# Kernel tuning notes

Hardware: AMD Instinct MI355X
Metric: run time of the kernel (lower is better)

The kernel has to match this reference:

```python
import jax, jax.numpy as jnp
import numpy as np

HEAD_DIM = 128
NUM_Q_HEAD = 32
NUM_KV_HEAD = 8
GROUP_SIZE = 128
EPS = 1e-5
WINDOW = 512
CAP = 50.0
CLIP_L, CLIP_R = -0.01, 1.01
SCALE = 1.0 / np.sqrt(HEAD_DIM)
NEG = -1e9


def group_rmsnorm(x, gamma, gsz, eps):
    # x: [B, S, H]; per-group RMS over contiguous chunks of size gsz, then learned scale
    b, s, h = x.shape
    xg = x.reshape(b, s, h // gsz, gsz)
    rms = jnp.sqrt(jnp.mean(xg * xg, axis=-1, keepdims=True) + eps)
    return (xg / rms).reshape(b, s, h) * gamma


def setup_inputs() -> dict:
    key = jax.random.key(0)
    k1, k2, k3, k4, k5 = jax.random.split(key, 5)
    B, S = 2, 2048
    q = jax.random.normal(k1, (B, S, NUM_Q_HEAD, HEAD_DIM), dtype=jnp.float32)
    k = jax.random.normal(k2, (B, S, NUM_KV_HEAD, HEAD_DIM), dtype=jnp.float32)
    v = jax.random.normal(k3, (B, S, NUM_KV_HEAD, HEAD_DIM), dtype=jnp.float32)
    # GroupRMSNorm weights ~ U(init_range) = U(-1, 1)
    gamma_q = jax.random.uniform(k4, (NUM_Q_HEAD * HEAD_DIM,), dtype=jnp.float32, minval=-1.0, maxval=1.0)
    gamma_k = jax.random.uniform(k5, (NUM_KV_HEAD * HEAD_DIM,), dtype=jnp.float32, minval=-1.0, maxval=1.0)
    return {"q": q, "k": k, "v": v, "gamma_q": gamma_q, "gamma_k": gamma_k}


def reference(q, k, v, gamma_q, gamma_k):
    B, Sq, Hq, D = q.shape
    Sk, Hkv = k.shape[1], k.shape[2]
    # QK GroupRMSNorm on flattened hidden dim
    qn = group_rmsnorm(q.reshape(B, Sq, Hq * D), gamma_q, GROUP_SIZE, EPS).reshape(B, Sq, Hq, D)
    kn = group_rmsnorm(k.reshape(B, Sk, Hkv * D), gamma_k, GROUP_SIZE, EPS).reshape(B, Sk, Hkv, D)
    # GQA: repeat_interleave kv heads to match q heads
    rep = Hq // Hkv
    kr = jnp.repeat(kn, rep, axis=2)
    vr = jnp.repeat(v, rep, axis=2)
    # scores: [B, H, Sq, Sk]
    logits = jnp.einsum('bqhd,bkhd->bhqk', qn, kr) * SCALE
    # softmax capping (temperature path skipped when cap is set)
    logits = jnp.tanh(logits / CAP) * CAP
    # causal + sliding-window mask (aligned at sequence end)
    i = jnp.arange(Sq)[:, None]
    j = jnp.arange(Sk)[None, :]
    pos = i + (Sk - Sq)
    allowed = (j <= pos) & (pos - j <= WINDOW)
    logits = jnp.where(allowed, logits, NEG)
    probs = jax.nn.softmax(logits.astype(jnp.float32), axis=-1)
    # softmax clipping: clamp(probs * (r - l) + l, 0, 1)
    probs = jnp.clip(probs * (CLIP_R - CLIP_L) + CLIP_L, 0.0, 1.0)
    # output: [B, Sq, H, D]
    o = jnp.einsum('bhqk,bkhd->bqhd', probs.astype(q.dtype), vr)
    return o
```

## Files before the change

kernel.cpp:

```cpp
#include <hip/hip_runtime.h>

#define SEQ     2048
#define NQH     32
#define NKV     8
#define HD      128
#define WINDOW  512
#define QT      64
#define EPS_F   1e-5f
#define CQ2     0.12752981793f
#define PSTR    72

#define QG      (2 * SEQ * NQH)
#define KG      (2 * SEQ * NKV)

#define QN_OFF  0
#define KN_OFF  33554432ull
#define VT_OFF  41943040ull

#define ROWPAT(r, hg) ((((r) & 3) + 8 * ((r) >> 2)) + 4 * (hg))

#define ASYNC_BAR() asm volatile("s_waitcnt vmcnt(0)\n\ts_barrier" ::: "memory")
#define LGKM_BAR()  asm volatile("s_waitcnt lgkmcnt(0)\n\ts_barrier" ::: "memory")

using bf16x8 = __attribute__((ext_vector_type(8))) __bf16;
using bf16x2 = __attribute__((ext_vector_type(2))) __bf16;
using f32x16 = __attribute__((ext_vector_type(16))) float;

__device__ __forceinline__ void dma16(const void* g, void* l) {
    __builtin_amdgcn_global_load_lds(
        (const __attribute__((address_space(1))) unsigned int*)g,
        (__attribute__((address_space(3))) unsigned int*)l, 16, 0, 0);
}

__global__ __launch_bounds__(256)
void prep(const float* __restrict__ q, const float* __restrict__ k,
          const float* __restrict__ v, const float* __restrict__ gq,
          const float* __restrict__ gk,
          __bf16* __restrict__ qn, __bf16* __restrict__ kn, __bf16* __restrict__ vt)
{
    __shared__ __align__(16) __bf16 tile[64 * 136];
    const int blk = blockIdx.x;
    const int tid = threadIdx.x;
    if (blk < 2048) {
        const int l16  = tid & 15;
        const int rsub = tid >> 4;
        #pragma unroll
        for (int it = 0; it < 5; it++) {
            const int row  = blk * 80 + it * 16 + rsub;
            const bool isq = row < QG;
            const int  kr  = row - QG;
            const float* src = isq ? (q + (size_t)row * HD) : (k + (size_t)kr * HD);
            const float* g   = isq ? (gq + (row & 31) * HD) : (gk + (kr & 7) * HD);
            float4 a  = *(const float4*)(src + l16 * 8);
            float4 b4 = *(const float4*)(src + l16 * 8 + 4);
            float ss = a.x*a.x + a.y*a.y + a.z*a.z + a.w*a.w
                     + b4.x*b4.x + b4.y*b4.y + b4.z*b4.z + b4.w*b4.w;
            ss += __shfl_xor(ss, 1); ss += __shfl_xor(ss, 2);
            ss += __shfl_xor(ss, 4); ss += __shfl_xor(ss, 8);
            const float rs = rsqrtf(ss * (1.f / 128.f) + EPS_F) * (isq ? CQ2 : 1.0f);
            float4 g0 = *(const float4*)(g + l16 * 8);
            float4 g1 = *(const float4*)(g + l16 * 8 + 4);
            bf16x8 o;
            o[0] = (__bf16)(a.x  * rs * g0.x);  o[1] = (__bf16)(a.y  * rs * g0.y);
            o[2] = (__bf16)(a.z  * rs * g0.z);  o[3] = (__bf16)(a.w  * rs * g0.w);
            o[4] = (__bf16)(b4.x * rs * g1.x);  o[5] = (__bf16)(b4.y * rs * g1.y);
            o[6] = (__bf16)(b4.z * rs * g1.z);  o[7] = (__bf16)(b4.w * rs * g1.w);
            __bf16* dst = (isq ? (qn + (size_t)row * HD) : (kn + (size_t)kr * HD)) + l16 * 8;
            *(bf16x8*)dst = o;
        }
    } else {
        const int blk2 = blk - 2048;
        const int st  = blk2 & 31;
        const int kvh = (blk2 >> 5) & 7;
        const int b   = blk2 >> 8;
        {
            const int r = tid >> 2, seg = (tid & 3) * 32;
            const float* src = v + ((size_t)(b * SEQ + st * 64 + r) * NKV + kvh) * HD + seg;
            #pragma unroll
            for (int u = 0; u < 4; u++) {
                float4 x = *(const float4*)(src + u * 8);
                float4 y = *(const float4*)(src + u * 8 + 4);
                bf16x8 w;
                w[0] = (__bf16)x.x; w[1] = (__bf16)x.y; w[2] = (__bf16)x.z; w[3] = (__bf16)x.w;
                w[4] = (__bf16)y.x; w[5] = (__bf16)y.y; w[6] = (__bf16)y.z; w[7] = (__bf16)y.w;
                *(bf16x8*)&tile[r * 136 + seg + u * 8] = w;
            }
        }
        __syncthreads();
        {
            const int d = tid >> 1, sp = (tid & 1) * 32;
            __bf16* dst = vt + ((size_t)(b * NKV + kvh) * HD + d) * SEQ + st * 64 + sp;
            #pragma unroll
            for (int u = 0; u < 32; u += 2) {
                bf16x2 p;
                p[0] = tile[(sp + u) * 136 + d];
                p[1] = tile[(sp + u + 1) * 136 + d];
                *(bf16x2*)(dst + u) = p;
            }
        }
    }
}

__global__ __launch_bounds__(256, 2)
void swa_main(const __bf16* __restrict__ qn, const __bf16* __restrict__ kn,
              const __bf16* __restrict__ vt, float* __restrict__ out)
{
    __shared__ __align__(16) __bf16 sK[2][QT * HD];
    __shared__ __align__(16) __bf16 sV[2][HD * 64];
    __shared__ __align__(16) __bf16 sP[QT * PSTR];
    __shared__ float sLp[2][QT];
    __shared__ float sInvL[QT];

    const int wg   = blockIdx.x;
    const int qt   = wg & 31;
    const int h    = (wg >> 5) & 31;
    const int b    = wg >> 10;
    const int kvh  = h >> 2;
    const int i0   = qt * QT;
    const int tid  = threadIdx.x;
    const int lane = tid & 63;
    const int wave = tid >> 6;
    const int mhalf = wave & 1;
    const int nhalf = wave >> 1;
    const int m    = lane & 31;
    const int hg   = lane >> 5;

    const char* k_src[4];  const char* q_src[4];  const char* v_src[4];
    int kq_off[4];  int v_off[4];
    {
        const char* kn_head = (const char*)kn + ((size_t)b * SEQ * NKV + kvh) * 256;
        const char* qn_head = (const char*)qn + (((size_t)(b * SEQ + i0)) * NQH + h) * 256;
        const char* vt_head = (const char*)vt + ((size_t)(b * NKV + kvh) * HD) * (SEQ * 2);
        #pragma unroll
        for (int i = 0; i < 4; i++) {
            const int chunk = wave * 4 + i;
            {
                const int r    = chunk * 4 + (lane >> 4);
                const int cpos = lane & 15;
                const int c    = (cpos & 8) | ((cpos ^ r) & 7);
                k_src[i]  = kn_head + (size_t)r * (NKV * HD * 2) + c * 16;
                q_src[i]  = qn_head + (size_t)r * (NQH * HD * 2) + c * 16;
                kq_off[i] = chunk * 1024;
            }
            {
                const int r    = chunk * 8 + (lane >> 3);
                const int cpos = lane & 7;
                const int c    = cpos ^ (r & 7);
                v_src[i] = vt_head + (size_t)r * (SEQ * 2) + c * 16;
                v_off[i] = chunk * 1024;
            }
        }
    }

    const int t_lo = (i0 >= WINDOW ? (i0 - WINDOW) : 0) >> 6;
    const int t_hi = i0 >> 6;
    const int krow = nhalf * 32 + m;

    #pragma unroll
    for (int i = 0; i < 4; i++) dma16(q_src[i], (char*)&sK[0][0] + kq_off[i]);
    __syncthreads();

    {
        const size_t ko = (size_t)t_lo * 64 * (NKV * HD * 2);
        #pragma unroll
        for (int i = 0; i < 4; i++) dma16(k_src[i] + ko, (char*)&sK[1][0] + kq_off[i]);
    }

    bf16x8 qf[8];
    {
        const int row = mhalf * 32 + m;
        #pragma unroll
        for (int kf = 0; kf < 8; kf++) {
            const int c   = kf * 2 + hg;
            const int pos = (c & 8) | ((c ^ row) & 7);
            qf[kf] = *(const bf16x8*)(&sK[0][0] + row * HD + pos * 8);
        }
    }

    float lacc[16];
    #pragma unroll
    for (int i = 0; i < 16; i++) lacc[i] = 0.f;

    int par = 1;
    for (int t = t_lo; t <= t_hi; t++) {
        ASYNC_BAR();
        if (t < t_hi) {
            const size_t ko = (size_t)(t + 1) * 64 * (NKV * HD * 2);
            #pragma unroll
            for (int i = 0; i < 4; i++) dma16(k_src[i] + ko, (char*)&sK[par ^ 1][0] + kq_off[i]);
        }
        const __bf16* kb = &sK[par][0];
        f32x16 c;
        #pragma unroll
        for (int i = 0; i < 16; i++) c[i] = 0.f;
        #pragma unroll
        for (int kf = 0; kf < 8; kf++) {
            const int cc  = kf * 2 + hg;
            const int pos = (cc & 8) | ((cc ^ krow) & 7);
            bf16x8 bk = *(const bf16x8*)(kb + krow * HD + pos * 8);
            c = __builtin_amdgcn_mfma_f32_32x32x16_bf16(qf[kf], bk, c, 0, 0, 0);
        }
        const bool do_mask = (t == t_hi) || (t == t_lo && i0 >= WINDOW);
        const int kj = t * 64 + krow;
        if (do_mask) {
            #pragma unroll
            for (int r = 0; r < 16; r++) {
                const int qi = i0 + mhalf * 32 + ROWPAT(r, hg);
                const float e = __builtin_amdgcn_exp2f(c[r]);
                lacc[r] += ((unsigned)(qi - kj) <= WINDOW) ? e : 0.f;
            }
        } else {
            #pragma unroll
            for (int r = 0; r < 16; r++) lacc[r] += __builtin_amdgcn_exp2f(c[r]);
        }
        par ^= 1;
    }

    #pragma unroll
    for (int r = 0; r < 16; r++) {
        float l = lacc[r];
        l += __shfl_xor(l, 1);  l += __shfl_xor(l, 2);  l += __shfl_xor(l, 4);
        l += __shfl_xor(l, 8);  l += __shfl_xor(l, 16);
        lacc[r] = l;
    }
    if (m == 0) {
        #pragma unroll
        for (int r = 0; r < 16; r++)
            sLp[nhalf][mhalf * 32 + ROWPAT(r, hg)] = lacc[r];
    }
    __syncthreads();
    if (tid < QT) sInvL[tid] = __builtin_amdgcn_rcpf(sLp[0][tid] + sLp[1][tid]);
    __syncthreads();

    float invl[16];
    #pragma unroll
    for (int r = 0; r < 16; r++) invl[r] = sInvL[mhalf * 32 + ROWPAT(r, hg)];

    f32x16 o0, o1;
    #pragma unroll
    for (int i = 0; i < 16; i++) { o0[i] = 0.f; o1[i] = 0.f; }

    {
        const size_t ko = (size_t)t_lo * 64 * (NKV * HD * 2);
        const size_t vo = (size_t)t_lo * 128;
        #pragma unroll
        for (int i = 0; i < 4; i++) {
            dma16(k_src[i] + ko, (char*)&sK[0][0] + kq_off[i]);
            dma16(v_src[i] + vo, (char*)&sV[0][0] + v_off[i]);
        }
    }
    par = 0;
    for (int t = t_lo; t <= t_hi; t++) {
        ASYNC_BAR();
        if (t < t_hi) {
            const size_t ko = (size_t)(t + 1) * 64 * (NKV * HD * 2);
            const size_t vo = (size_t)(t + 1) * 128;
            #pragma unroll
            for (int i = 0; i < 4; i++) {
                dma16(k_src[i] + ko, (char*)&sK[par ^ 1][0] + kq_off[i]);
                dma16(v_src[i] + vo, (char*)&sV[par ^ 1][0] + v_off[i]);
            }
        }
        const __bf16* kb = &sK[par][0];
        const __bf16* vb = &sV[par][0];

        f32x16 c;
        #pragma unroll
        for (int i = 0; i < 16; i++) c[i] = 0.f;
        #pragma unroll
        for (int kf = 0; kf < 8; kf++) {
            const int cc  = kf * 2 + hg;
            const int pos = (cc & 8) | ((cc ^ krow) & 7);
            bf16x8 bk = *(const bf16x8*)(kb + krow * HD + pos * 8);
            c = __builtin_amdgcn_mfma_f32_32x32x16_bf16(qf[kf], bk, c, 0, 0, 0);
        }
        const bool do_mask = (t == t_hi) || (t == t_lo && i0 >= WINDOW);
        const int kj = t * 64 + krow;
        #pragma unroll
        for (int r = 0; r < 16; r++) {
            const int row = mhalf * 32 + ROWPAT(r, hg);
            const float p = __builtin_amdgcn_exp2f(c[r]) * invl[r];
            float f = fminf(fmaxf(fmaf(p, 1.02f, -0.01f), 0.f), 1.f);
            if (do_mask) {
                const int qi = i0 + row;
                f = ((unsigned)(qi - kj) <= WINDOW) ? f : 0.f;
            }
            sP[row * PSTR + krow] = (__bf16)f;
        }
        LGKM_BAR();

        bf16x8 pa[4];
        #pragma unroll
        for (int kf = 0; kf < 4; kf++)
            pa[kf] = *(const bf16x8*)&sP[(mhalf * 32 + m) * PSTR + kf * 16 + hg * 8];
        #pragma unroll
        for (int kf = 0; kf < 4; kf++) {
            const int cc = kf * 2 + hg;
            {
                const int row = nhalf * 64 + m;
                bf16x8 v0 = *(const bf16x8*)(vb + row * 64 + ((cc ^ row) & 7) * 8);
                o0 = __builtin_amdgcn_mfma_f32_32x32x16_bf16(pa[kf], v0, o0, 0, 0, 0);
            }
            {
                const int row = nhalf * 64 + 32 + m;
                bf16x8 v1 = *(const bf16x8*)(vb + row * 64 + ((cc ^ row) & 7) * 8);
                o1 = __builtin_amdgcn_mfma_f32_32x32x16_bf16(pa[kf], v1, o1, 0, 0, 0);
            }
        }
        par ^= 1;
    }

    #pragma unroll
    for (int r = 0; r < 16; r++) {
        const int row = i0 + mhalf * 32 + ROWPAT(r, hg);
        float* op = out + ((size_t)(b * SEQ + row) * NQH + h) * HD + nhalf * 64 + m;
        op[0]  = o0[r];
        op[32] = o1[r];
    }
}

extern "C" void kernel_launch(void* const* d_in, const int* in_sizes, int n_in,
                              void* d_out, int out_size, void* d_ws, size_t ws_size,
                              hipStream_t stream) {
    const float* q  = (const float*)d_in[0];
    const float* k  = (const float*)d_in[1];
    const float* v  = (const float*)d_in[2];
    const float* gq = (const float*)d_in[3];
    const float* gk = (const float*)d_in[4];
    float* out = (float*)d_out;

    __bf16* qn = (__bf16*)((char*)d_ws + QN_OFF);
    __bf16* kn = (__bf16*)((char*)d_ws + KN_OFF);
    __bf16* vt = (__bf16*)((char*)d_ws + VT_OFF);

    prep<<<2560, 256, 0, stream>>>(q, k, v, gq, gk, qn, kn, vt);
    swa_main<<<2 * NQH * (SEQ / QT), 256, 0, stream>>>(qn, kn, vt, out);
}
```

Before: 248.1 us.

## Fuse Q RMSNorm into attention, cache exponentials in registers, drop K recompute

Q normalization moves out of the prep kernel and into the attention kernel, which reads fp32 q straight from global memory. This removes the bf16 qn round trip through workspace. The second pass no longer reloads K and recomputes QK^T: the first pass keeps the exponentials in registers (9 tiles × 2 bf16x8) and the second pass only streams V. The V transpose in prep is reworked, and the K and V shared buffers are merged. The trade is much higher register pressure and bf16 rounding of the unnormalised exponentials before clipping, which could affect occupancy and accuracy.

```diff
diff --git a/kernel.cpp b/kernel.cpp
--- a/kernel.cpp
+++ b/kernel.cpp
@@ -10,12 +10,8 @@
 #define CQ2     0.12752981793f
 #define PSTR    72
 
-#define QG      (2 * SEQ * NQH)
-#define KG      (2 * SEQ * NKV)
-
-#define QN_OFF  0
-#define KN_OFF  33554432ull
-#define VT_OFF  41943040ull
+#define KN_OFF  0ull
+#define VT_OFF  8388608ull
 
 #define ROWPAT(r, hg) ((((r) & 3) + 8 * ((r) >> 2)) + 4 * (hg))
 
@@ -23,7 +19,6 @@
 #define LGKM_BAR()  asm volatile("s_waitcnt lgkmcnt(0)\n\ts_barrier" ::: "memory")
 
 using bf16x8 = __attribute__((ext_vector_type(8))) __bf16;
-using bf16x2 = __attribute__((ext_vector_type(2))) __bf16;
 using f32x16 = __attribute__((ext_vector_type(16))) float;
 
 __device__ __forceinline__ void dma16(const void* g, void* l) {
@@ -33,80 +28,78 @@
 }
 
 __global__ __launch_bounds__(256)
-void prep(const float* __restrict__ q, const float* __restrict__ k,
-          const float* __restrict__ v, const float* __restrict__ gq,
+void prep(const float* __restrict__ k, const float* __restrict__ v,
           const float* __restrict__ gk,
-          __bf16* __restrict__ qn, __bf16* __restrict__ kn, __bf16* __restrict__ vt)
+          __bf16* __restrict__ kn, __bf16* __restrict__ vt)
 {
-    __shared__ __align__(16) __bf16 tile[64 * 136];
+    __shared__ __align__(16) __bf16 sT[HD * 72];
     const int blk = blockIdx.x;
     const int tid = threadIdx.x;
-    if (blk < 2048) {
+    if (blk < 512) {
         const int l16  = tid & 15;
         const int rsub = tid >> 4;
         #pragma unroll
-        for (int it = 0; it < 5; it++) {
-            const int row  = blk * 80 + it * 16 + rsub;
-            const bool isq = row < QG;
-            const int  kr  = row - QG;
-            const float* src = isq ? (q + (size_t)row * HD) : (k + (size_t)kr * HD);
-            const float* g   = isq ? (gq + (row & 31) * HD) : (gk + (kr & 7) * HD);
-            float4 a  = *(const float4*)(src + l16 * 8);
-            float4 b4 = *(const float4*)(src + l16 * 8 + 4);
+        for (int it = 0; it < 4; it++) {
+            const int row = blk * 64 + it * 16 + rsub;
+            const float* src = k + (size_t)row * HD + l16 * 8;
+            const float* g   = gk + (row & 7) * HD + l16 * 8;
+            float4 a  = *(const float4*)(src);
+            float4 b4 = *(const float4*)(src + 4);
             float ss = a.x*a.x + a.y*a.y + a.z*a.z + a.w*a.w
                      + b4.x*b4.x + b4.y*b4.y + b4.z*b4.z + b4.w*b4.w;
             ss += __shfl_xor(ss, 1); ss += __shfl_xor(ss, 2);
             ss += __shfl_xor(ss, 4); ss += __shfl_xor(ss, 8);
-            const float rs = rsqrtf(ss * (1.f / 128.f) + EPS_F) * (isq ? CQ2 : 1.0f);
-            float4 g0 = *(const float4*)(g + l16 * 8);
-            float4 g1 = *(const float4*)(g + l16 * 8 + 4);
+            const float rs = rsqrtf(ss * (1.f / 128.f) + EPS_F);
+            float4 g0 = *(const float4*)(g);
+            float4 g1 = *(const float4*)(g + 4);
             bf16x8 o;
             o[0] = (__bf16)(a.x  * rs * g0.x);  o[1] = (__bf16)(a.y  * rs * g0.y);
             o[2] = (__bf16)(a.z  * rs * g0.z);  o[3] = (__bf16)(a.w  * rs * g0.w);
             o[4] = (__bf16)(b4.x * rs * g1.x);  o[5] = (__bf16)(b4.y * rs * g1.y);
             o[6] = (__bf16)(b4.z * rs * g1.z);  o[7] = (__bf16)(b4.w * rs * g1.w);
-            __bf16* dst = (isq ? (qn + (size_t)row * HD) : (kn + (size_t)kr * HD)) + l16 * 8;
-            *(bf16x8*)dst = o;
+            *(bf16x8*)(kn + (size_t)row * HD + l16 * 8) = o;
         }
     } else {
-        const int blk2 = blk - 2048;
+        const int blk2 = blk - 512;
         const int st  = blk2 & 31;
         const int kvh = (blk2 >> 5) & 7;
         const int b   = blk2 >> 8;
+        const int s0  = st * 64;
         {
-            const int r = tid >> 2, seg = (tid & 3) * 32;
-            const float* src = v + ((size_t)(b * SEQ + st * 64 + r) * NKV + kvh) * HD + seg;
-            #pragma unroll
-            for (int u = 0; u < 4; u++) {
-                float4 x = *(const float4*)(src + u * 8);
-                float4 y = *(const float4*)(src + u * 8 + 4);
-                bf16x8 w;
-                w[0] = (__bf16)x.x; w[1] = (__bf16)x.y; w[2] = (__bf16)x.z; w[3] = (__bf16)x.w;
-                w[4] = (__bf16)y.x; w[5] = (__bf16)y.y; w[6] = (__bf16)y.z; w[7] = (__bf16)y.w;
-                *(bf16x8*)&tile[r * 136 + seg + u * 8] = w;
+            const int r  = tid >> 2;
+            const int q4 = tid & 3;
+            const float* src = v + ((size_t)(b * SEQ + s0 + r) * NKV + kvh) * HD;
+            #pragma unroll
+            for (int u = 0; u < 8; u++) {
+                const int d0 = q4 * 4 + u * 16;
+                float4 x = *(const float4*)(src + d0);
+                sT[(d0 + 0) * 72 + r] = (__bf16)x.x;
+                sT[(d0 + 1) * 72 + r] = (__bf16)x.y;
+                sT[(d0 + 2) * 72 + r] = (__bf16)x.z;
+                sT[(d0 + 3) * 72 + r] = (__bf16)x.w;
             }
         }
         __syncthreads();
         {
-            const int d = tid >> 1, sp = (tid & 1) * 32;
-            __bf16* dst = vt + ((size_t)(b * NKV + kvh) * HD + d) * SEQ + st * 64 + sp;
-            #pragma unroll
-            for (int u = 0; u < 32; u += 2) {
-                bf16x2 p;
-                p[0] = tile[(sp + u) * 136 + d];
-                p[1] = tile[(sp + u + 1) * 136 + d];
-                *(bf16x2*)(dst + u) = p;
+            const int c     = tid & 7;
+            const int dbase = tid >> 3;
+            __bf16* dst = vt + ((size_t)(b * NKV + kvh) * HD) * SEQ + s0;
+            #pragma unroll
+            for (int i = 0; i < 4; i++) {
+                const int d = dbase + i * 32;
+                bf16x8 w = *(const bf16x8*)&sT[d * 72 + c * 8];
+                *(bf16x8*)(dst + (size_t)d * SEQ + c * 8) = w;
             }
         }
     }
 }
 
 __global__ __launch_bounds__(256, 2)
-void swa_main(const __bf16* __restrict__ qn, const __bf16* __restrict__ kn,
-              const __bf16* __restrict__ vt, float* __restrict__ out)
+void swa_main(const float* __restrict__ q, const __bf16* __restrict__ kn,
+              const __bf16* __restrict__ vt, const float* __restrict__ gq,
+              float* __restrict__ out)
 {
-    __shared__ __align__(16) __bf16 sK[2][QT * HD];
-    __shared__ __align__(16) __bf16 sV[2][HD * 64];
+    __shared__ __align__(16) __bf16 sKV[2][QT * HD];
     __shared__ __align__(16) __bf16 sP[QT * PSTR];
     __shared__ float sLp[2][QT];
     __shared__ float sInvL[QT];
@@ -125,11 +118,10 @@
     const int m    = lane & 31;
     const int hg   = lane >> 5;
 
-    const char* k_src[4];  const char* q_src[4];  const char* v_src[4];
+    const char* k_src[4];  const char* v_src[4];
     int kq_off[4];  int v_off[4];
     {
         const char* kn_head = (const char*)kn + ((size_t)b * SEQ * NKV + kvh) * 256;
-        const char* qn_head = (const char*)qn + (((size_t)(b * SEQ + i0)) * NQH + h) * 256;
         const char* vt_head = (const char*)vt + ((size_t)(b * NKV + kvh) * HD) * (SEQ * 2);
         #pragma unroll
         for (int i = 0; i < 4; i++) {
@@ -139,7 +131,6 @@
                 const int cpos = lane & 15;
                 const int c    = (cpos & 8) | ((cpos ^ r) & 7);
                 k_src[i]  = kn_head + (size_t)r * (NKV * HD * 2) + c * 16;
-                q_src[i]  = qn_head + (size_t)r * (NQH * HD * 2) + c * 16;
                 kq_off[i] = chunk * 1024;
             }
             {
@@ -152,68 +143,103 @@
         }
     }
 
-    const int t_lo = (i0 >= WINDOW ? (i0 - WINDOW) : 0) >> 6;
-    const int t_hi = i0 >> 6;
-    const int krow = nhalf * 32 + m;
-
-    #pragma unroll
-    for (int i = 0; i < 4; i++) dma16(q_src[i], (char*)&sK[0][0] + kq_off[i]);
-    __syncthreads();
+    const int t_lo   = (i0 >= WINDOW ? (i0 - WINDOW) : 0) >> 6;
+    const int t_hi   = i0 >> 6;
+    const int ttbias = t_hi - 8;
+    const int krow   = nhalf * 32 + m;
 
     {
         const size_t ko = (size_t)t_lo * 64 * (NKV * HD * 2);
-        #pragma unroll
-        for (int i = 0; i < 4; i++) dma16(k_src[i] + ko, (char*)&sK[1][0] + kq_off[i]);
+        const int p0 = (t_lo - ttbias) & 1;
+        #pragma unroll
+        for (int i = 0; i < 4; i++) dma16(k_src[i] + ko, (char*)&sKV[p0][0] + kq_off[i]);
     }
 
     bf16x8 qf[8];
     {
-        const int row = mhalf * 32 + m;
+        const int qrow = i0 + mhalf * 32 + m;
+        const float* qp = q + ((size_t)(b * SEQ + qrow) * NQH + h) * HD;
+        float4 qb[16];
+        float ss = 0.0f;
         #pragma unroll
         for (int kf = 0; kf < 8; kf++) {
-            const int c   = kf * 2 + hg;
-            const int pos = (c & 8) | ((c ^ row) & 7);
-            qf[kf] = *(const bf16x8*)(&sK[0][0] + row * HD + pos * 8);
+            const int d0 = kf * 16 + hg * 8;
+            float4 a  = *(const float4*)(qp + d0);
+            float4 b4 = *(const float4*)(qp + d0 + 4);
+            qb[kf * 2] = a; qb[kf * 2 + 1] = b4;
+            ss += a.x*a.x + a.y*a.y + a.z*a.z + a.w*a.w
+                + b4.x*b4.x + b4.y*b4.y + b4.z*b4.z + b4.w*b4.w;
+        }
+        ss += __shfl_xor(ss, 32);
+        const float rs = rsqrtf(ss * (1.f / 128.f) + EPS_F) * CQ2;
+        const float* gp = gq + h * HD;
+        #pragma unroll
+        for (int kf = 0; kf < 8; kf++) {
+            const int d0 = kf * 16 + hg * 8;
+            float4 g0 = *(const float4*)(gp + d0);
+            float4 g1 = *(const float4*)(gp + d0 + 4);
+            bf16x8 f;
+            f[0] = (__bf16)(qb[kf*2].x   * rs * g0.x);
+            f[1] = (__bf16)(qb[kf*2].y   * rs * g0.y);
+            f[2] = (__bf16)(qb[kf*2].z   * rs * g0.z);
+            f[3] = (__bf16)(qb[kf*2].w   * rs * g0.w);
+            f[4] = (__bf16)(qb[kf*2+1].x * rs * g1.x);
+            f[5] = (__bf16)(qb[kf*2+1].y * rs * g1.y);
+            f[6] = (__bf16)(qb[kf*2+1].z * rs * g1.z);
+            f[7] = (__bf16)(qb[kf*2+1].w * rs * g1.w);
+            qf[kf] = f;
         }
     }
 
     float lacc[16];
     #pragma unroll
     for (int i = 0; i < 16; i++) lacc[i] = 0.f;
-
-    int par = 1;
-    for (int t = t_lo; t <= t_hi; t++) {
-        ASYNC_BAR();
-        if (t < t_hi) {
-            const size_t ko = (size_t)(t + 1) * 64 * (NKV * HD * 2);
-            #pragma unroll
-            for (int i = 0; i < 4; i++) dma16(k_src[i] + ko, (char*)&sK[par ^ 1][0] + kq_off[i]);
-        }
-        const __bf16* kb = &sK[par][0];
-        f32x16 c;
-        #pragma unroll
-        for (int i = 0; i < 16; i++) c[i] = 0.f;
-        #pragma unroll
-        for (int kf = 0; kf < 8; kf++) {
-            const int cc  = kf * 2 + hg;
-            const int pos = (cc & 8) | ((cc ^ krow) & 7);
-            bf16x8 bk = *(const bf16x8*)(kb + krow * HD + pos * 8);
-            c = __builtin_amdgcn_mfma_f32_32x32x16_bf16(qf[kf], bk, c, 0, 0, 0);
-        }
-        const bool do_mask = (t == t_hi) || (t == t_lo && i0 >= WINDOW);
-        const int kj = t * 64 + krow;
-        if (do_mask) {
+    bf16x8 ec[9][2];
+
+    #pragma unroll
+    for (int tt = 0; tt < 9; tt++) {
+        const int t = ttbias + tt;
+        if (t >= t_lo) {
+            ASYNC_BAR();
+            const __bf16* kb = &sKV[tt & 1][0];
+            bf16x8 bk[8];
+            #pragma unroll
+            for (int kf = 0; kf < 8; kf++) {
+                const int cc  = kf * 2 + hg;
+                const int pos = (cc & 8) | ((cc ^ krow) & 7);
+                bk[kf] = *(const bf16x8*)(kb + krow * HD + pos * 8);
+            }
+            if (t < t_hi) {
+                const size_t ko = (size_t)(t + 1) * 64 * (NKV * HD * 2);
+                #pragma unroll
+                for (int i = 0; i < 4; i++)
+                    dma16(k_src[i] + ko, (char*)&sKV[(tt + 1) & 1][0] + kq_off[i]);
+            }
+            f32x16 c;
+            #pragma unroll
+            for (int i = 0; i < 16; i++) c[i] = 0.f;
+            #pragma unroll
+            for (int kf = 0; kf < 8; kf++)
+                c = __builtin_amdgcn_mfma_f32_32x32x16_bf16(qf[kf], bk[kf], c, 0, 0, 0);
+
+            const bool do_mask = (t == t_hi) || (t == t_lo && i0 >= WINDOW);
+            const int kj = t * 64 + krow;
+            float e[16];
             #pragma unroll
             for (int r = 0; r < 16; r++) {
-                const int qi = i0 + mhalf * 32 + ROWPAT(r, hg);
-                const float e = __builtin_amdgcn_exp2f(c[r]);
-                lacc[r] += ((unsigned)(qi - kj) <= WINDOW) ? e : 0.f;
-            }
-        } else {
-            #pragma unroll
-            for (int r = 0; r < 16; r++) lacc[r] += __builtin_amdgcn_exp2f(c[r]);
-        }
-        par ^= 1;
+                float ev = __builtin_amdgcn_exp2f(c[r]);
+                if (do_mask) {
+                    const int qi = i0 + mhalf * 32 + ROWPAT(r, hg);
+                    ev = ((unsigned)(qi - kj) <= WINDOW) ? ev : 0.f;
+                }
+                lacc[r] += ev;
+                e[r] = ev;
+            }
+            bf16x8 p0v, p1v;
+            #pragma unroll
+            for (int j = 0; j < 8; j++) { p0v[j] = (__bf16)e[j]; p1v[j] = (__bf16)e[8 + j]; }
+            ec[tt][0] = p0v;  ec[tt][1] = p1v;
+        }
     }
 
     #pragma unroll
@@ -232,82 +258,60 @@
     if (tid < QT) sInvL[tid] = __builtin_amdgcn_rcpf(sLp[0][tid] + sLp[1][tid]);
     __syncthreads();
 
-    float invl[16];
-    #pragma unroll
-    for (int r = 0; r < 16; r++) invl[r] = sInvL[mhalf * 32 + ROWPAT(r, hg)];
+    float ar[16];
+    #pragma unroll
+    for (int r = 0; r < 16; r++) ar[r] = 1.02f * sInvL[mhalf * 32 + ROWPAT(r, hg)];
+
+    {
+        const size_t vo = (size_t)t_lo * 128;
+        const int p0 = (t_lo - ttbias) & 1;
+        #pragma unroll
+        for (int i = 0; i < 4; i++) dma16(v_src[i] + vo, (char*)&sKV[p0][0] + v_off[i]);
+    }
 
     f32x16 o0, o1;
     #pragma unroll
     for (int i = 0; i < 16; i++) { o0[i] = 0.f; o1[i] = 0.f; }
 
-    {
-        const size_t ko = (size_t)t_lo * 64 * (NKV * HD * 2);
-        const size_t vo = (size_t)t_lo * 128;
-        #pragma unroll
-        for (int i = 0; i < 4; i++) {
-            dma16(k_src[i] + ko, (char*)&sK[0][0] + kq_off[i]);
-            dma16(v_src[i] + vo, (char*)&sV[0][0] + v_off[i]);
-        }
-    }
-    par = 0;
-    for (int t = t_lo; t <= t_hi; t++) {
-        ASYNC_BAR();
-        if (t < t_hi) {
-            const size_t ko = (size_t)(t + 1) * 64 * (NKV * HD * 2);
-            const size_t vo = (size_t)(t + 1) * 128;
-            #pragma unroll
-            for (int i = 0; i < 4; i++) {
-                dma16(k_src[i] + ko, (char*)&sK[par ^ 1][0] + kq_off[i]);
-                dma16(v_src[i] + vo, (char*)&sV[par ^ 1][0] + v_off[i]);
-            }
-        }
-        const __bf16* kb = &sK[par][0];
-        const __bf16* vb = &sV[par][0];
-
-        f32x16 c;
-        #pragma unroll
-        for (int i = 0; i < 16; i++) c[i] = 0.f;
-        #pragma unroll
-        for (int kf = 0; kf < 8; kf++) {
-            const int cc  = kf * 2 + hg;
-            const int pos = (cc & 8) | ((cc ^ krow) & 7);
-            bf16x8 bk = *(const bf16x8*)(kb + krow * HD + pos * 8);
-            c = __builtin_amdgcn_mfma_f32_32x32x16_bf16(qf[kf], bk, c, 0, 0, 0);
-        }
-        const bool do_mask = (t == t_hi) || (t == t_lo && i0 >= WINDOW);
-        const int kj = t * 64 + krow;
-        #pragma unroll
-        for (int r = 0; r < 16; r++) {
-            const int row = mhalf * 32 + ROWPAT(r, hg);
-            const float p = __builtin_amdgcn_exp2f(c[r]) * invl[r];
-            float f = fminf(fmaxf(fmaf(p, 1.02f, -0.01f), 0.f), 1.f);
-            if (do_mask) {
-                const int qi = i0 + row;
-                f = ((unsigned)(qi - kj) <= WINDOW) ? f : 0.f;
-            }
-            sP[row * PSTR + krow] = (__bf16)f;
-        }
-        LGKM_BAR();
-
-        bf16x8 pa[4];
-        #pragma unroll
-        for (int kf = 0; kf < 4; kf++)
-            pa[kf] = *(const bf16x8*)&sP[(mhalf * 32 + m) * PSTR + kf * 16 + hg * 8];
-        #pragma unroll
-        for (int kf = 0; kf < 4; kf++) {
-            const int cc = kf * 2 + hg;
-            {
-                const int row = nhalf * 64 + m;
-                bf16x8 v0 = *(const bf16x8*)(vb + row * 64 + ((cc ^ row) & 7) * 8);
-                o0 = __builtin_amdgcn_mfma_f32_32x32x16_bf16(pa[kf], v0, o0, 0, 0, 0);
-            }
-            {
-                const int row = nhalf * 64 + 32 + m;
-                bf16x8 v1 = *(const bf16x8*)(vb + row * 64 + ((cc ^ row) & 7) * 8);
-                o1 = __builtin_amdgcn_mfma_f32_32x32x16_bf16(pa[kf], v1, o1, 0, 0, 0);
-            }
-        }
-        par ^= 1;
+    #pragma unroll
+    for (int tt = 0; tt < 9; tt++) {
+        const int t = ttbias + tt;
+        if (t >= t_lo) {
+            ASYNC_BAR();
+            #pragma unroll
+            for (int half = 0; half < 2; half++) {
+                #pragma unroll
+                for (int j = 0; j < 8; j++) {
+                    const int r = half * 8 + j;
+                    const float ee = (float)ec[tt][half][j];
+                    const float f = fminf(fmaxf(fmaf(ee, ar[r], -0.01f), 0.f), 1.f);
+                    sP[(mhalf * 32 + ROWPAT(r, hg)) * PSTR + krow] = (__bf16)f;
+                }
+            }
+            LGKM_BAR();
+            const __bf16* vb = &sKV[tt & 1][0];
+            bf16x8 pa[4], vf0[4], vf1[4];
+            #pragma unroll
+            for (int kf = 0; kf < 4; kf++) {
+                pa[kf] = *(const bf16x8*)&sP[(mhalf * 32 + m) * PSTR + kf * 16 + hg * 8];
+                const int cc = kf * 2 + hg;
+                const int row0 = nhalf * 64 + m;
+                const int row1 = nhalf * 64 + 32 + m;
+                vf0[kf] = *(const bf16x8*)(vb + row0 * 64 + ((cc ^ row0) & 7) * 8);
+                vf1[kf] = *(const bf16x8*)(vb + row1 * 64 + ((cc ^ row1) & 7) * 8);
+            }
+            if (t < t_hi) {
+                const size_t vo = (size_t)(t + 1) * 128;
+                #pragma unroll
+                for (int i = 0; i < 4; i++)
+                    dma16(v_src[i] + vo, (char*)&sKV[(tt + 1) & 1][0] + v_off[i]);
+            }
+            #pragma unroll
+            for (int kf = 0; kf < 4; kf++) {
+                o0 = __builtin_amdgcn_mfma_f32_32x32x16_bf16(pa[kf], vf0[kf], o0, 0, 0, 0);
+                o1 = __builtin_amdgcn_mfma_f32_32x32x16_bf16(pa[kf], vf1[kf], o1, 0, 0, 0);
+            }
+        }
     }
 
     #pragma unroll
@@ -329,10 +333,9 @@
     const float* gk = (const float*)d_in[4];
     float* out = (float*)d_out;
 
-    __bf16* qn = (__bf16*)((char*)d_ws + QN_OFF);
     __bf16* kn = (__bf16*)((char*)d_ws + KN_OFF);
     __bf16* vt = (__bf16*)((char*)d_ws + VT_OFF);
 
-    prep<<<2560, 256, 0, stream>>>(q, k, v, gq, gk, qn, kn, vt);
-    swa_main<<<2 * NQH * (SEQ / QT), 256, 0, stream>>>(qn, kn, vt, out);
+    prep<<<1024, 256, 0, stream>>>(k, v, gk, kn, vt);
+    swa_main<<<2 * NQH * (SEQ / QT), 256, 0, stream>>>(q, kn, vt, gq, out);
 }
```

Measured after the change: 219.4 us. 1.13x faster.
